# Performance work log

Hardware: AMD Instinct MI355X
Metric: run time of the kernel (lower is better)

The kernel has to match this reference:

```python
import jax, jax.numpy as jnp
import numpy as np

C_IN = 256


def setup_inputs() -> dict:
    key = jax.random.key(0)
    ks = jax.random.split(key, 10)
    B, C, H, W = 1, C_IN, 96, 96
    Cq = C // 8
    s = 0.05
    return {
        "x": jax.random.normal(ks[0], (B, C, H, W), dtype=jnp.float32),
        "Wq": jax.random.normal(ks[1], (Cq, C), dtype=jnp.float32) * s,
        "bq": jax.random.normal(ks[2], (Cq,), dtype=jnp.float32) * s,
        "Wk": jax.random.normal(ks[3], (Cq, C), dtype=jnp.float32) * s,
        "bk": jax.random.normal(ks[4], (Cq,), dtype=jnp.float32) * s,
        "Wv": jax.random.normal(ks[5], (C, C), dtype=jnp.float32) * s,
        "bv": jax.random.normal(ks[6], (C,), dtype=jnp.float32) * s,
        "W6": jax.random.normal(ks[7], (C, C), dtype=jnp.float32) * s,
        "b6": jax.random.normal(ks[8], (C,), dtype=jnp.float32) * s,
        "gamma": jnp.ones((1,), dtype=jnp.float32),
    }


def reference(x, Wq, bq, Wk, bk, Wv, bv, W6, b6, gamma):
    # TRM forward (OFS just wraps it). 1x1 convs expressed as einsums.
    B, C, H, W = x.shape
    N = H * W
    scale = C ** -0.5  # 1 / sqrt(in_dim)
    xf = x.reshape(B, C, N)
    q = jnp.einsum('oc,bcn->bon', Wq, xf) + bq[None, :, None]   # (B, C/8, N)
    k = jnp.einsum('oc,bcn->bon', Wk, xf) + bk[None, :, None]   # (B, C/8, N)
    v = jnp.einsum('oc,bcn->bon', Wv, xf) + bv[None, :, None]   # (B, C,   N)
    # energy[b,n,m] = sum_c q[b,c,n] * k[b,c,m]  -> full spatial attention (B,N,N)
    energy = jnp.einsum('bcn,bcm->bnm', q, k)
    att = jax.nn.softmax(energy, axis=-1)
    # out[b,c,n] = sum_m v[b,c,m] * att[b,n,m]
    out = jnp.einsum('bcm,bnm->bcn', v, att)                    # (B, C, N)
    # torch: out.permute(2,0,1) -> (N,B,C); max/mean over C; sum; mean over B
    out_co = out.max(axis=1) + out.mean(axis=1)                 # (B, N)
    x_co = out_co.mean(axis=0).reshape(B, -1) * scale           # valid because B == 1
    x_co = jax.nn.softmax(x_co, axis=-1).reshape(B, 1, H, W)    # spatial gate
    gated = x * x_co
    y = jnp.einsum('oc,bchw->bohw', W6, gated) + b6[None, :, None, None]
    return gamma * y + x + y
```

## Files before the change

### kernel.cpp

```cpp
#include <hip/hip_runtime.h>

#define N 9216
#define CIN 256
#define DQ 32
#define NT 144
#define LOG2E 1.44269504088896340736f

typedef short short8 __attribute__((ext_vector_type(8)));
typedef float floatx4 __attribute__((ext_vector_type(4)));
typedef unsigned short ushort_t;

__device__ __forceinline__ ushort_t f2bf(float f) {
  union { float f; unsigned u; } a; a.f = f;
  unsigned u = a.u;
  u += 0x7fffu + ((u >> 16) & 1u);
  return (ushort_t)(u >> 16);
}
__device__ __forceinline__ ushort_t f2bf_fast(float f) {
  union { float f; unsigned u; } a; a.f = f;
  return (ushort_t)((a.u + 0x8000u) >> 16);
}
__device__ __forceinline__ float bf2f(ushort_t h) {
  union { unsigned u; float f; } a; a.u = ((unsigned)h) << 16;
  return a.f;
}

#define ACC4(R, W, XV)                                                   \
  acc[R][0] += (W) * (XV).x;  acc[R][1] += (W) * (XV).y;                 \
  acc[R][2] += (W) * (XV).z;  acc[R][3] += (W) * (XV).w;

__global__ __launch_bounds__(256) void qkv_kernel(
    const float* __restrict__ x,
    const float* __restrict__ Wq, const float* __restrict__ bq,
    const float* __restrict__ Wk, const float* __restrict__ bk,
    const float* __restrict__ Wv, const float* __restrict__ bv,
    ushort_t* __restrict__ qT, ushort_t* __restrict__ kT,
    ushort_t* __restrict__ vG)
{
  __shared__ float xs[64][68];
  const int t = threadIdx.x;
  const int n0 = blockIdx.x * 64;
  const int oc = blockIdx.y;
  const int i = t >> 4, j = t & 15;
  const int o0 = oc * 64 + i * 4;

  const float *W0, *W1, *W2, *W3;
  float b0, b1, b2, b3;
  {
    const int o = o0;
    if (oc == 0) {
      if (o < 32) { W0 = Wq + o*CIN; W1 = Wq + (o+1)*CIN; W2 = Wq + (o+2)*CIN; W3 = Wq + (o+3)*CIN;
                    b0 = bq[o]; b1 = bq[o+1]; b2 = bq[o+2]; b3 = bq[o+3]; }
      else        { W0 = Wk + (o-32)*CIN; W1 = Wk + (o-31)*CIN; W2 = Wk + (o-30)*CIN; W3 = Wk + (o-29)*CIN;
                    b0 = bk[o-32]; b1 = bk[o-31]; b2 = bk[o-30]; b3 = bk[o-29]; }
    } else        { W0 = Wv + (o-64)*CIN; W1 = Wv + (o-63)*CIN; W2 = Wv + (o-62)*CIN; W3 = Wv + (o-61)*CIN;
                    b0 = bv[o-64]; b1 = bv[o-63]; b2 = bv[o-62]; b3 = bv[o-61]; }
  }

  float acc[4][4] = {};
  for (int cc = 0; cc < 4; ++cc) {
    {
      const int row = t >> 2, cq = t & 3;
      const float* src = x + (size_t)(cc * 64 + row) * N + n0 + cq * 16;
      float4 a0 = *(const float4*)(src + 0);
      float4 a1 = *(const float4*)(src + 4);
      float4 a2 = *(const float4*)(src + 8);
      float4 a3 = *(const float4*)(src + 12);
      float* dst = &xs[row][cq * 16];
      *(float4*)(dst + 0) = a0; *(float4*)(dst + 4)  = a1;
      *(float4*)(dst + 8) = a2; *(float4*)(dst + 12) = a3;
    }
    __syncthreads();
#pragma unroll 4
    for (int k4 = 0; k4 < 16; ++k4) {
      const float4 w0 = *(const float4*)(W0 + cc * 64 + k4 * 4);
      const float4 w1 = *(const float4*)(W1 + cc * 64 + k4 * 4);
      const float4 w2 = *(const float4*)(W2 + cc * 64 + k4 * 4);
      const float4 w3 = *(const float4*)(W3 + cc * 64 + k4 * 4);
      const float4 x0 = *(const float4*)&xs[k4 * 4 + 0][j * 4];
      const float4 x1 = *(const float4*)&xs[k4 * 4 + 1][j * 4];
      const float4 x2 = *(const float4*)&xs[k4 * 4 + 2][j * 4];
      const float4 x3 = *(const float4*)&xs[k4 * 4 + 3][j * 4];
      ACC4(0, w0.x, x0) ACC4(0, w0.y, x1) ACC4(0, w0.z, x2) ACC4(0, w0.w, x3)
      ACC4(1, w1.x, x0) ACC4(1, w1.y, x1) ACC4(1, w1.z, x2) ACC4(1, w1.w, x3)
      ACC4(2, w2.x, x0) ACC4(2, w2.y, x1) ACC4(2, w2.z, x2) ACC4(2, w2.w, x3)
      ACC4(3, w3.x, x0) ACC4(3, w3.y, x1) ACC4(3, w3.z, x2) ACC4(3, w3.w, x3)
    }
    __syncthreads();
  }

  const float bias[4] = {b0, b1, b2, b3};
#pragma unroll
  for (int r = 0; r < 4; ++r) {
    const int o = o0 + r;
#pragma unroll
    for (int c = 0; c < 4; ++c) {
      const int n = n0 + j * 4 + c;
      const float val = acc[r][c] + bias[r];
      if (oc == 0) {
        if (o < 32) qT[(size_t)n * DQ + o]        = f2bf(val * LOG2E);
        else        kT[(size_t)n * DQ + (o - 32)] = f2bf(val);
      } else        vG[(size_t)(o - 64) * N + n]  = f2bf(val);
    }
  }
}

__global__ __launch_bounds__(256, 4) void attn_kernel(
    const ushort_t* __restrict__ qT, const ushort_t* __restrict__ kT,
    const ushort_t* __restrict__ vG,
    ushort_t* __restrict__ Opart, float* __restrict__ lpart,
    int base, int rem)
{
  __shared__ ushort_t Pb[2][64][36];

  const int t = threadIdx.x;
  const int w = t >> 6;
  const int lane = t & 63;
  const int quad = lane >> 4;
  const int l15 = lane & 15;
  const int nt = blockIdx.x;
  const int s  = blockIdx.y;
  const int n0 = nt * 64;
  const int sliceIters = base + (s < rem ? 1 : 0);
  const int it0 = s * base + (s < rem ? s : rem);
  const int mbase = it0 * 32;
  const int cw = w * 64;

  short8 aq = *(const short8*)(qT + (size_t)(n0 + 16 * w + l15) * DQ + 8 * quad);

  floatx4 acc[4][4];
#pragma unroll
  for (int a2 = 0; a2 < 4; ++a2)
#pragma unroll
    for (int b2 = 0; b2 < 4; ++b2)
      acc[a2][b2] = (floatx4){0.f, 0.f, 0.f, 0.f};
  float lsum[4] = {0.f, 0.f, 0.f, 0.f};
  const floatx4 z4 = {0.f, 0.f, 0.f, 0.f};

  for (int it = 0; it < sliceIters; ++it) {
    const int m0 = mbase + it * 32;

    short8 kb0 = *(const short8*)(kT + (size_t)(m0 + l15) * DQ + 8 * quad);
    short8 kb1 = *(const short8*)(kT + (size_t)(m0 + 16 + l15) * DQ + 8 * quad);
    floatx4 s0 = __builtin_amdgcn_mfma_f32_16x16x32_bf16(aq, kb0, z4, 0, 0, 0);
    floatx4 s1 = __builtin_amdgcn_mfma_f32_16x16x32_bf16(aq, kb1, z4, 0, 0, 0);

    const ushort_t* vb = vG + (size_t)m0 + 8 * quad;
    short8 av0 = *(const short8*)(vb + (size_t)(cw +  0 + l15) * N);
    short8 av1 = *(const short8*)(vb + (size_t)(cw + 16 + l15) * N);
    short8 av2 = *(const short8*)(vb + (size_t)(cw + 32 + l15) * N);
    short8 av3 = *(const short8*)(vb + (size_t)(cw + 48 + l15) * N);

    ushort_t* pb = &Pb[it & 1][0][0];
#pragma unroll
    for (int r = 0; r < 4; ++r) {
      float p0 = exp2f(s0[r]);
      float p1 = exp2f(s1[r]);
      lsum[r] += p0 + p1;
      const int row = 16 * w + 4 * quad + r;
      pb[row * 36 + l15]      = f2bf_fast(p0);
      pb[row * 36 + 16 + l15] = f2bf_fast(p1);
    }
    __syncthreads();

#pragma unroll
    for (int b2 = 0; b2 < 4; ++b2) {
      const ushort_t* pr = pb + (b2 * 16 + l15) * 36 + 8 * quad;
      union { uint2 u2[2]; short8 v; } u;
      u.u2[0] = *(const uint2*)(pr);
      u.u2[1] = *(const uint2*)(pr + 4);
      const short8 pf = u.v;
      acc[0][b2] = __builtin_amdgcn_mfma_f32_16x16x32_bf16(av0, pf, acc[0][b2], 0, 0, 0);
      acc[1][b2] = __builtin_amdgcn_mfma_f32_16x16x32_bf16(av1, pf, acc[1][b2], 0, 0, 0);
      acc[2][b2] = __builtin_amdgcn_mfma_f32_16x16x32_bf16(av2, pf, acc[2][b2], 0, 0, 0);
      acc[3][b2] = __builtin_amdgcn_mfma_f32_16x16x32_bf16(av3, pf, acc[3][b2], 0, 0, 0);
    }
  }

#pragma unroll
  for (int r = 0; r < 4; ++r) {
    float v = lsum[r];
    v += __shfl_xor(v, 1);
    v += __shfl_xor(v, 2);
    v += __shfl_xor(v, 4);
    v += __shfl_xor(v, 8);
    lsum[r] = v;
  }
  if (l15 == 0) {
#pragma unroll
    for (int r = 0; r < 4; ++r)
      lpart[(size_t)s * N + n0 + 16 * w + 4 * quad + r] = lsum[r];
  }

  const size_t basep = ((size_t)s * NT + nt) * 256;
#pragma unroll
  for (int a2 = 0; a2 < 4; ++a2)
#pragma unroll
    for (int b2 = 0; b2 < 4; ++b2)
#pragma unroll
      for (int r = 0; r < 4; ++r) {
        const int c  = cw + a2 * 16 + 4 * quad + r;
        const int nl = b2 * 16 + l15;
        Opart[(basep + c) * 64 + nl] = f2bf(acc[a2][b2][r]);
      }
}

template<int NSL>
__global__ __launch_bounds__(256) void cco_partial(
    const ushort_t* __restrict__ Opart,
    float* __restrict__ pmax, float* __restrict__ psum)
{
  const int nt = blockIdx.x, cy = blockIdx.y;
  const int t = threadIdx.x;
  const int n = t & 63, ci = t >> 6;
  float mx = -3.4e38f, sm = 0.f;
#pragma unroll
  for (int k = 0; k < 8; ++k) {
    const int c = cy * 32 + ci + 4 * k;
    float val = 0.f;
#pragma unroll
    for (int s2 = 0; s2 < NSL; ++s2)
      val += bf2f(Opart[(((size_t)s2 * NT + nt) * 256 + c) * 64 + n]);
    mx = fmaxf(mx, val);
    sm += val;
  }
  __shared__ float rmx[4][64], rsm[4][64];
  rmx[ci][n] = mx; rsm[ci][n] = sm;
  __syncthreads();
  if (t < 64) {
    const float m2 = fmaxf(fmaxf(rmx[0][t], rmx[1][t]), fmaxf(rmx[2][t], rmx[3][t]));
    const float s2 = rsm[0][t] + rsm[1][t] + rsm[2][t] + rsm[3][t];
    pmax[(size_t)cy * N + nt * 64 + t] = m2;
    psum[(size_t)cy * N + nt * 64 + t] = s2;
  }
}

template<int NSL>
__global__ __launch_bounds__(256) void cco_final(
    const float* __restrict__ pmax, const float* __restrict__ psum,
    const float* __restrict__ lpart, float* __restrict__ out_co)
{
  const int n = blockIdx.x * 256 + threadIdx.x;
  float m = -3.4e38f, s = 0.f, l = 0.f;
#pragma unroll
  for (int g = 0; g < 8; ++g) {
    m = fmaxf(m, pmax[(size_t)g * N + n]);
    s += psum[(size_t)g * N + n];
  }
#pragma unroll
  for (int s3 = 0; s3 < NSL; ++s3) l += lpart[(size_t)s3 * N + n];
  out_co[n] = (m + s * (1.0f / 256.0f)) / l;
}

__global__ __launch_bounds__(1024) void gate_kernel(
    const float* __restrict__ out_co, float* __restrict__ x_co)
{
  const int t = threadIdx.x;
  float z[9];
#pragma unroll
  for (int i2 = 0; i2 < 9; ++i2) z[i2] = out_co[t + 1024 * i2] * 0.0625f;
  float mx = z[0];
#pragma unroll
  for (int i2 = 1; i2 < 9; ++i2) mx = fmaxf(mx, z[i2]);
  for (int off = 32; off > 0; off >>= 1) mx = fmaxf(mx, __shfl_xor(mx, off));
  __shared__ float redm[16], reds[16];
  const int wv = t >> 6, ln = t & 63;
  if (ln == 0) redm[wv] = mx;
  __syncthreads();
  mx = redm[0];
#pragma unroll
  for (int i2 = 1; i2 < 16; ++i2) mx = fmaxf(mx, redm[i2]);

  float e[9]; float sm = 0.f;
#pragma unroll
  for (int i2 = 0; i2 < 9; ++i2) { e[i2] = exp2f((z[i2] - mx) * LOG2E); sm += e[i2]; }
  for (int off = 32; off > 0; off >>= 1) sm += __shfl_xor(sm, off);
  if (ln == 0) reds[wv] = sm;
  __syncthreads();
  sm = 0.f;
#pragma unroll
  for (int i2 = 0; i2 < 16; ++i2) sm += reds[i2];
  const float inv = 1.0f / sm;
#pragma unroll
  for (int i2 = 0; i2 < 9; ++i2) x_co[t + 1024 * i2] = e[i2] * inv;
}

__global__ __launch_bounds__(256) void final_kernel(
    const float* __restrict__ x, const float* __restrict__ W6,
    const float* __restrict__ b6, const float* __restrict__ gamma,
    const float* __restrict__ x_co, float* __restrict__ out)
{
  __shared__ float xs[64][68];
  const int t = threadIdx.x;
  const int n0 = blockIdx.x * 64;
  const int i = t >> 4, j = t & 15;
  const int o0 = blockIdx.y * 64 + i * 4;

  const float* W0 = W6 + (size_t)(o0 + 0) * CIN;
  const float* W1 = W6 + (size_t)(o0 + 1) * CIN;
  const float* W2 = W6 + (size_t)(o0 + 2) * CIN;
  const float* W3 = W6 + (size_t)(o0 + 3) * CIN;

  float acc[4][4] = {};
  for (int cc = 0; cc < 4; ++cc) {
    {
      const int row = t >> 2, cq = t & 3;
      const float* src = x + (size_t)(cc * 64 + row) * N + n0 + cq * 16;
      float4 a0 = *(const float4*)(src + 0);
      float4 a1 = *(const float4*)(src + 4);
      float4 a2 = *(const float4*)(src + 8);
      float4 a3 = *(const float4*)(src + 12);
      float* dst = &xs[row][cq * 16];
      *(float4*)(dst + 0) = a0; *(float4*)(dst + 4)  = a1;
      *(float4*)(dst + 8) = a2; *(float4*)(dst + 12) = a3;
    }
    __syncthreads();
#pragma unroll 4
    for (int k4 = 0; k4 < 16; ++k4) {
      const float4 w0 = *(const float4*)(W0 + cc * 64 + k4 * 4);
      const float4 w1 = *(const float4*)(W1 + cc * 64 + k4 * 4);
      const float4 w2 = *(const float4*)(W2 + cc * 64 + k4 * 4);
      const float4 w3 = *(const float4*)(W3 + cc * 64 + k4 * 4);
      const float4 x0 = *(const float4*)&xs[k4 * 4 + 0][j * 4];
      const float4 x1 = *(const float4*)&xs[k4 * 4 + 1][j * 4];
      const float4 x2 = *(const float4*)&xs[k4 * 4 + 2][j * 4];
      const float4 x3 = *(const float4*)&xs[k4 * 4 + 3][j * 4];
      ACC4(0, w0.x, x0) ACC4(0, w0.y, x1) ACC4(0, w0.z, x2) ACC4(0, w0.w, x3)
      ACC4(1, w1.x, x0) ACC4(1, w1.y, x1) ACC4(1, w1.z, x2) ACC4(1, w1.w, x3)
      ACC4(2, w2.x, x0) ACC4(2, w2.y, x1) ACC4(2, w2.z, x2) ACC4(2, w2.w, x3)
      ACC4(3, w3.x, x0) ACC4(3, w3.y, x1) ACC4(3, w3.z, x2) ACC4(3, w3.w, x3)
    }
    __syncthreads();
  }

  const float g1 = 1.0f + gamma[0];
  const float4 xc = *(const float4*)(x_co + n0 + j * 4);
#pragma unroll
  for (int r = 0; r < 4; ++r) {
    const int o = o0 + r;
    const float bv6 = b6[o];
    const float4 xrow = *(const float4*)(x + (size_t)o * N + n0 + j * 4);
    float4 res;
    res.x = xrow.x + g1 * (xc.x * acc[r][0] + bv6);
    res.y = xrow.y + g1 * (xc.y * acc[r][1] + bv6);
    res.z = xrow.z + g1 * (xc.z * acc[r][2] + bv6);
    res.w = xrow.w + g1 * (xc.w * acc[r][3] + bv6);
    *(float4*)(out + (size_t)o * N + n0 + j * 4) = res;
  }
}

extern "C" void kernel_launch(void* const* d_in, const int* in_sizes, int n_in,
                              void* d_out, int out_size, void* d_ws, size_t ws_size,
                              hipStream_t stream)
{
  const float* x     = (const float*)d_in[0];
  const float* Wq    = (const float*)d_in[1];
  const float* bq    = (const float*)d_in[2];
  const float* Wk    = (const float*)d_in[3];
  const float* bk    = (const float*)d_in[4];
  const float* Wv    = (const float*)d_in[5];
  const float* bv    = (const float*)d_in[6];
  const float* W6    = (const float*)d_in[7];
  const float* b6    = (const float*)d_in[8];
  const float* gamma = (const float*)d_in[9];
  float* out = (float*)d_out;

  const size_t fixed = (size_t)N * DQ * 2 * 2
                     + (size_t)CIN * N * 2
                     + (size_t)N * 4 * 2
                     + (size_t)8 * N * 4 * 2;
  int nsl = 7;
  size_t need = fixed + (size_t)nsl * NT * 256 * 64 * 2 + (size_t)nsl * N * 4;
  if (ws_size < need) nsl = 4;
  const int totIters = N / 32;
  const int base = totIters / nsl;
  const int rem  = totIters % nsl;

  char* ws = (char*)d_ws;
  const size_t OFF_QT = 0;
  const size_t OFF_KT = OFF_QT + (size_t)N * DQ * 2;
  const size_t OFF_V  = OFF_KT + (size_t)N * DQ * 2;
  const size_t OFF_OP = OFF_V  + (size_t)CIN * N * 2;
  const size_t OFF_LP = OFF_OP + (size_t)nsl * NT * 256 * 64 * 2;
  const size_t OFF_PM = OFF_LP + (size_t)nsl * N * 4;
  const size_t OFF_PS = OFF_PM + (size_t)8 * N * 4;
  const size_t OFF_OC = OFF_PS + (size_t)8 * N * 4;
  const size_t OFF_XC = OFF_OC + (size_t)N * 4;

  ushort_t* qT     = (ushort_t*)(ws + OFF_QT);
  ushort_t* kT     = (ushort_t*)(ws + OFF_KT);
  ushort_t* vG     = (ushort_t*)(ws + OFF_V);
  ushort_t* Opart  = (ushort_t*)(ws + OFF_OP);
  float*    lpart  = (float*)(ws + OFF_LP);
  float*    pmax   = (float*)(ws + OFF_PM);
  float*    psum   = (float*)(ws + OFF_PS);
  float*    out_co = (float*)(ws + OFF_OC);
  float*    x_co   = (float*)(ws + OFF_XC);

  qkv_kernel<<<dim3(NT, 5), 256, 0, stream>>>(x, Wq, bq, Wk, bk, Wv, bv, qT, kT, vG);
  attn_kernel<<<dim3(NT, nsl), 256, 0, stream>>>(qT, kT, vG, Opart, lpart, base, rem);
  if (nsl == 7) {
    cco_partial<7><<<dim3(NT, 8), 256, 0, stream>>>(Opart, pmax, psum);
    cco_final<7><<<N / 256, 256, 0, stream>>>(pmax, psum, lpart, out_co);
  } else {
    cco_partial<4><<<dim3(NT, 8), 256, 0, stream>>>(Opart, pmax, psum);
    cco_final<4><<<N / 256, 256, 0, stream>>>(pmax, psum, lpart, out_co);
  }
  gate_kernel<<<1, 1024, 0, stream>>>(out_co, x_co);
  final_kernel<<<dim3(NT, 4), 256, 0, stream>>>(x, W6, b6, gamma, x_co, out);
}
```

Measured before the change: 246.4 us.

## Fuse channel reduction, normalization and spatial softmax into one kernel with atomic sum

Merges cco_partial, cco_final and gate_kernel into a single 1024-thread-per-tile kernel. It reduces all 256 channels per spatial tile, computes the exponentials without max subtraction, and accumulates the global exp-sum with one atomicAdd per block. The final kernel now applies the 1/sum normalization itself, and the sum is zeroed in qkv_kernel. This removes two launches, the single-block gate kernel and the intermediate buffers. In exchange, softmax drops max subtraction, which risks overflow for large inputs, and the float atomics make the summation order nondeterministic.

```diff
diff --git a/kernel.cpp b/kernel.cpp
--- a/kernel.cpp
+++ b/kernel.cpp
@@ -35,8 +35,10 @@
     const float* __restrict__ Wk, const float* __restrict__ bk,
     const float* __restrict__ Wv, const float* __restrict__ bv,
     ushort_t* __restrict__ qT, ushort_t* __restrict__ kT,
-    ushort_t* __restrict__ vG)
-{
+    ushort_t* __restrict__ vG, float* __restrict__ sumExp)
+{
+  if (blockIdx.x == 0 && blockIdx.y == 0 && threadIdx.x == 0) *sumExp = 0.f;
+
   __shared__ float xs[64][68];
   const int t = threadIdx.x;
   const int n0 = blockIdx.x * 64;
@@ -206,17 +208,17 @@
 }
 
 template<int NSL>
-__global__ __launch_bounds__(256) void cco_partial(
-    const ushort_t* __restrict__ Opart,
-    float* __restrict__ pmax, float* __restrict__ psum)
-{
-  const int nt = blockIdx.x, cy = blockIdx.y;
+__global__ __launch_bounds__(1024) void cco_kernel(
+    const ushort_t* __restrict__ Opart, const float* __restrict__ lpart,
+    float* __restrict__ e_buf, float* __restrict__ sumExp)
+{
+  const int nt = blockIdx.x;
   const int t = threadIdx.x;
   const int n = t & 63, ci = t >> 6;
   float mx = -3.4e38f, sm = 0.f;
 #pragma unroll
-  for (int k = 0; k < 8; ++k) {
-    const int c = cy * 32 + ci + 4 * k;
+  for (int k = 0; k < 16; ++k) {
+    const int c = ci * 16 + k;
     float val = 0.f;
 #pragma unroll
     for (int s2 = 0; s2 < NSL; ++s2)
@@ -224,71 +226,32 @@
     mx = fmaxf(mx, val);
     sm += val;
   }
-  __shared__ float rmx[4][64], rsm[4][64];
+  __shared__ float rmx[16][64], rsm[16][64];
   rmx[ci][n] = mx; rsm[ci][n] = sm;
   __syncthreads();
   if (t < 64) {
-    const float m2 = fmaxf(fmaxf(rmx[0][t], rmx[1][t]), fmaxf(rmx[2][t], rmx[3][t]));
-    const float s2 = rsm[0][t] + rsm[1][t] + rsm[2][t] + rsm[3][t];
-    pmax[(size_t)cy * N + nt * 64 + t] = m2;
-    psum[(size_t)cy * N + nt * 64 + t] = s2;
-  }
-}
-
-template<int NSL>
-__global__ __launch_bounds__(256) void cco_final(
-    const float* __restrict__ pmax, const float* __restrict__ psum,
-    const float* __restrict__ lpart, float* __restrict__ out_co)
-{
-  const int n = blockIdx.x * 256 + threadIdx.x;
-  float m = -3.4e38f, s = 0.f, l = 0.f;
-#pragma unroll
-  for (int g = 0; g < 8; ++g) {
-    m = fmaxf(m, pmax[(size_t)g * N + n]);
-    s += psum[(size_t)g * N + n];
-  }
-#pragma unroll
-  for (int s3 = 0; s3 < NSL; ++s3) l += lpart[(size_t)s3 * N + n];
-  out_co[n] = (m + s * (1.0f / 256.0f)) / l;
-}
-
-__global__ __launch_bounds__(1024) void gate_kernel(
-    const float* __restrict__ out_co, float* __restrict__ x_co)
-{
-  const int t = threadIdx.x;
-  float z[9];
-#pragma unroll
-  for (int i2 = 0; i2 < 9; ++i2) z[i2] = out_co[t + 1024 * i2] * 0.0625f;
-  float mx = z[0];
-#pragma unroll
-  for (int i2 = 1; i2 < 9; ++i2) mx = fmaxf(mx, z[i2]);
-  for (int off = 32; off > 0; off >>= 1) mx = fmaxf(mx, __shfl_xor(mx, off));
-  __shared__ float redm[16], reds[16];
-  const int wv = t >> 6, ln = t & 63;
-  if (ln == 0) redm[wv] = mx;
-  __syncthreads();
-  mx = redm[0];
-#pragma unroll
-  for (int i2 = 1; i2 < 16; ++i2) mx = fmaxf(mx, redm[i2]);
-
-  float e[9]; float sm = 0.f;
-#pragma unroll
-  for (int i2 = 0; i2 < 9; ++i2) { e[i2] = exp2f((z[i2] - mx) * LOG2E); sm += e[i2]; }
-  for (int off = 32; off > 0; off >>= 1) sm += __shfl_xor(sm, off);
-  if (ln == 0) reds[wv] = sm;
-  __syncthreads();
-  sm = 0.f;
-#pragma unroll
-  for (int i2 = 0; i2 < 16; ++i2) sm += reds[i2];
-  const float inv = 1.0f / sm;
-#pragma unroll
-  for (int i2 = 0; i2 < 9; ++i2) x_co[t + 1024 * i2] = e[i2] * inv;
+    float m = rmx[0][t], s = rsm[0][t];
+#pragma unroll
+    for (int g = 1; g < 16; ++g) { m = fmaxf(m, rmx[g][t]); s += rsm[g][t]; }
+    float l = 0.f;
+#pragma unroll
+    for (int s3 = 0; s3 < NSL; ++s3) l += lpart[(size_t)s3 * N + nt * 64 + t];
+    const float oc = (m + s * (1.0f / 256.0f)) / l;
+    const float ev = exp2f(oc * (0.0625f * LOG2E));
+    e_buf[nt * 64 + t] = ev;
+    float vs = ev;
+    vs += __shfl_xor(vs, 1);  vs += __shfl_xor(vs, 2);
+    vs += __shfl_xor(vs, 4);  vs += __shfl_xor(vs, 8);
+    vs += __shfl_xor(vs, 16); vs += __shfl_xor(vs, 32);
+    if (t == 0) atomicAdd(sumExp, vs);
+  }
 }
 
 __global__ __launch_bounds__(256) void final_kernel(
     const float* __restrict__ x, const float* __restrict__ W6,
     const float* __restrict__ b6, const float* __restrict__ gamma,
-    const float* __restrict__ x_co, float* __restrict__ out)
+    const float* __restrict__ e_buf, const float* __restrict__ sumExp,
+    float* __restrict__ out)
 {
   __shared__ float xs[64][68];
   const int t = threadIdx.x;
@@ -334,7 +297,9 @@
   }
 
   const float g1 = 1.0f + gamma[0];
-  const float4 xc = *(const float4*)(x_co + n0 + j * 4);
+  const float inv = 1.0f / sumExp[0];
+  float4 xc = *(const float4*)(e_buf + n0 + j * 4);
+  xc.x *= inv; xc.y *= inv; xc.z *= inv; xc.w *= inv;
 #pragma unroll
   for (int r = 0; r < 4; ++r) {
     const int o = o0 + r;
@@ -367,8 +332,8 @@
 
   const size_t fixed = (size_t)N * DQ * 2 * 2
                      + (size_t)CIN * N * 2
-                     + (size_t)N * 4 * 2
-                     + (size_t)8 * N * 4 * 2;
+                     + (size_t)N * 4
+                     + 256;
   int nsl = 7;
   size_t need = fixed + (size_t)nsl * NT * 256 * 64 * 2 + (size_t)nsl * N * 4;
   if (ws_size < need) nsl = 4;
@@ -382,30 +347,20 @@
   const size_t OFF_V  = OFF_KT + (size_t)N * DQ * 2;
   const size_t OFF_OP = OFF_V  + (size_t)CIN * N * 2;
   const size_t OFF_LP = OFF_OP + (size_t)nsl * NT * 256 * 64 * 2;
-  const size_t OFF_PM = OFF_LP + (size_t)nsl * N * 4;
-  const size_t OFF_PS = OFF_PM + (size_t)8 * N * 4;
-  const size_t OFF_OC = OFF_PS + (size_t)8 * N * 4;
-  const size_t OFF_XC = OFF_OC + (size_t)N * 4;
+  const size_t OFF_EB = OFF_LP + (size_t)nsl * N * 4;
+  const size_t OFF_SE = OFF_EB + (size_t)N * 4;
 
   ushort_t* qT     = (ushort_t*)(ws + OFF_QT);
   ushort_t* kT     = (ushort_t*)(ws + OFF_KT);
   ushort_t* vG     = (ushort_t*)(ws + OFF_V);
   ushort_t* Opart  = (ushort_t*)(ws + OFF_OP);
   float*    lpart  = (float*)(ws + OFF_LP);
-  float*    pmax   = (float*)(ws + OFF_PM);
-  float*    psum   = (float*)(ws + OFF_PS);
-  float*    out_co = (float*)(ws + OFF_OC);
-  float*    x_co   = (float*)(ws + OFF_XC);
-
-  qkv_kernel<<<dim3(NT, 5), 256, 0, stream>>>(x, Wq, bq, Wk, bk, Wv, bv, qT, kT, vG);
+  float*    e_buf  = (float*)(ws + OFF_EB);
+  float*    sumExp = (float*)(ws + OFF_SE);
+
+  qkv_kernel<<<dim3(NT, 5), 256, 0, stream>>>(x, Wq, bq, Wk, bk, Wv, bv, qT, kT, vG, sumExp);
   attn_kernel<<<dim3(NT, nsl), 256, 0, stream>>>(qT, kT, vG, Opart, lpart, base, rem);
-  if (nsl == 7) {
-    cco_partial<7><<<dim3(NT, 8), 256, 0, stream>>>(Opart, pmax, psum);
-    cco_final<7><<<N / 256, 256, 0, stream>>>(pmax, psum, lpart, out_co);
-  } else {
-    cco_partial<4><<<dim3(NT, 8), 256, 0, stream>>>(Opart, pmax, psum);
-    cco_final<4><<<N / 256, 256, 0, stream>>>(pmax, psum, lpart, out_co);
-  }
-  gate_kernel<<<1, 1024, 0, stream>>>(out_co, x_co);
-  final_kernel<<<dim3(NT, 4), 256, 0, stream>>>(x, W6, b6, gamma, x_co, out);
-}
+  if (nsl == 7) cco_kernel<7><<<NT, 1024, 0, stream>>>(Opart, lpart, e_buf, sumExp);
+  else          cco_kernel<4><<<NT, 1024, 0, stream>>>(Opart, lpart, e_buf, sumExp);
+  final_kernel<<<dim3(NT, 4), 256, 0, stream>>>(x, W6, b6, gamma, e_buf, sumExp, out);
+}
```

New measurement: 244.0 us. No clear change (-1.0%).
